# Performance work log

Hardware: AMD Instinct MI355X
Metric: run time of the kernel (lower is better)

The kernel has to match this reference:

```python
import jax, jax.numpy as jnp
import numpy as np

N = 50000   # nodes
E = 800000  # directed edges
D = 128     # input_channels


def _kaiming(key, shape):
    fan_in = shape[0]
    return jax.random.normal(key, shape, jnp.float32) * np.float32(np.sqrt(2.0 / fan_in))


def setup_inputs():
    key = jax.random.key(0)
    ks = jax.random.split(key, 8)
    x = jax.random.normal(ks[0], (N, D), jnp.float32)
    edge_index = jax.random.randint(ks[1], (2, E), 0, N, dtype=jnp.int32)
    return {
        "x": x,
        "edge_index": edge_index,
        "W_in": _kaiming(ks[2], (D, D)),      "b_in": jnp.zeros((D,), jnp.float32),
        "W1": _kaiming(ks[3], (D, 2 * D)),    "b1": jnp.zeros((2 * D,), jnp.float32),
        "W2": _kaiming(ks[4], (2 * D, D)),    "b2": jnp.zeros((D,), jnp.float32),
        "W3": _kaiming(ks[5], (D, D // 2)),   "b3": jnp.zeros((D // 2,), jnp.float32),
        "W_out": _kaiming(ks[6], (D // 2, 1)), "b_out": jnp.zeros((1,), jnp.float32),
    }


def _gcn_conv(x, src, dst, W, b, n):
    """PyG GCNConv: add self-loops, symmetric D^-1/2 (A+I) D^-1/2 normalization."""
    h = x @ W  # [n, out]
    loop = jnp.arange(n, dtype=src.dtype)
    s = jnp.concatenate([src, loop])  # message sources (x_j)
    d = jnp.concatenate([dst, loop])  # aggregation targets (x_i)
    deg = jax.ops.segment_sum(jnp.ones_like(d, jnp.float32), d, num_segments=n)
    dis = jnp.where(deg > 0, jax.lax.rsqrt(jnp.maximum(deg, 1.0)), 0.0)
    norm = dis[s] * dis[d]  # [E+n]
    msg = h[s] * norm[:, None]  # gather + scale
    out = jax.ops.segment_sum(msg, d, num_segments=n)  # scatter-add
    return out + b


def reference(x, edge_index, W_in, b_in, W1, b1, W2, b2, W3, b3, W_out, b_out):
    src, dst = edge_index[0], edge_index[1]
    n = x.shape[0]
    lrelu = lambda t: jax.nn.leaky_relu(t, 0.01)
    # dropout in eval mode (identity)
    h = lrelu(x @ W_in + b_in)
    h = lrelu(_gcn_conv(h, src, dst, W1, b1, n))
    h = lrelu(_gcn_conv(h, src, dst, W2, b2, n))
    h = lrelu(_gcn_conv(h, src, dst, W3, b3, n))
    return h @ W_out + b_out  # [n, 1]
```

## Files before the change

### kernel.cpp

```cpp
#include <hip/hip_runtime.h>
#include <hip/hip_cooperative_groups.h>

namespace cg = cooperative_groups;


#define LRELU(v) ((v) > 0.f ? (v) : 0.01f * (v))

typedef __attribute__((ext_vector_type(8))) _Float16 half8;
typedef __attribute__((ext_vector_type(8))) float float8;
typedef __attribute__((ext_vector_type(4))) float floatx4;

constexpr int CAP = 64;
constexpr int SMEM_H = 16896;

template <int K, int F, int EPI, int CG, int KG, typename IT>
__device__ void phase_gemm(const IT* __restrict__ X,
                           const _Float16* __restrict__ Wt,
                           const float* __restrict__ b,
                           const int* __restrict__ cnt,
                           _Float16* __restrict__ out, int M,
                           _Float16* xs) {
  constexpr int TM = 64;
  constexpr int LK = K + 8;
  constexpr int CW = F / 4;
  constexpr int CPW = CW / CG;
  constexpr int NT = CPW / 16;
  constexpr int KH = K / KG;
  constexpr int NKg = KH / 32;

  const int tid = threadIdx.x;
  const int w = tid >> 6;
  const int lane = tid & 63;
  const int m = lane & 15;
  const int q = lane >> 4;
  const int nTiles = (M + TM - 1) / TM;

  for (int tile = blockIdx.x; tile < nTiles; tile += gridDim.x) {
    const int m0 = tile * TM;
    __syncthreads();
    constexpr int CPR = K / 8;
    for (int idx = tid; idx < TM * CPR; idx += 256) {
      const int row = idx / CPR;
      const int kk = idx % CPR;
      const int g = m0 + row;
      half8 h = (half8)(_Float16)0.f;
      if (g < M) {
        if constexpr (sizeof(IT) == 4) {
          const float4* p = (const float4*)&X[(long)g * K + kk * 8];
          float4 a = p[0], c = p[1];
          h[0] = (_Float16)a.x; h[1] = (_Float16)a.y;
          h[2] = (_Float16)a.z; h[3] = (_Float16)a.w;
          h[4] = (_Float16)c.x; h[5] = (_Float16)c.y;
          h[6] = (_Float16)c.z; h[7] = (_Float16)c.w;
        } else {
          h = *(const half8*)&X[(long)g * K + kk * 8];
        }
      }
      *(half8*)&xs[row * LK + kk * 8] = h;
    }
    __syncthreads();

    for (int cg = 0; cg < CG; ++cg) {
      const int colbase = w * CW + cg * CPW;
      floatx4 acc[4][NT];
#pragma unroll
      for (int rt = 0; rt < 4; ++rt)
#pragma unroll
        for (int t = 0; t < NT; ++t) acc[rt][t] = (floatx4){0.f, 0.f, 0.f, 0.f};

      for (int kg = 0; kg < KG; ++kg) {
        half8 breg[NT][NKg];
#pragma unroll
        for (int t = 0; t < NT; ++t)
#pragma unroll
          for (int kc = 0; kc < NKg; ++kc)
            breg[t][kc] = *(const half8*)&Wt[(long)(colbase + t * 16 + m) * K +
                                             kg * KH + kc * 32 + q * 8];
#pragma unroll
        for (int kc = 0; kc < NKg; ++kc) {
          half8 af[4];
#pragma unroll
          for (int rt = 0; rt < 4; ++rt)
            af[rt] = *(const half8*)&xs[(rt * 16 + m) * LK + kg * KH + kc * 32 +
                                        q * 8];
#pragma unroll
          for (int rt = 0; rt < 4; ++rt)
#pragma unroll
            for (int t = 0; t < NT; ++t)
              acc[rt][t] = __builtin_amdgcn_mfma_f32_16x16x32_f16(
                  af[rt], breg[t][kc], acc[rt][t], 0, 0, 0);
        }
      }

#pragma unroll
      for (int rt = 0; rt < 4; ++rt) {
#pragma unroll
        for (int r = 0; r < 4; ++r) {
          const int row = m0 + rt * 16 + q * 4 + r;
          if (row < M) {
            const float dv = rsqrtf((float)cnt[row] + 1.0f);
#pragma unroll
            for (int t = 0; t < NT; ++t) {
              const int col = colbase + t * 16 + m;
              float v = acc[rt][t][r];
              if constexpr (EPI == 0) { v += b[col]; v = LRELU(v); v *= dv; }
              if constexpr (EPI == 1) { v += b[col]; v = LRELU(v); }
              if constexpr (EPI == 2) { v *= dv; }
              out[(long)row * F + col] = (_Float16)v;
            }
          }
        }
      }
    }
  }
}

template <int F, int MODE>
__device__ void phase_agg(const _Float16* __restrict__ G,
                          const unsigned short* __restrict__ pad,
                          const int* __restrict__ cnt,
                          const float* __restrict__ b,
                          const float* __restrict__ Wout,
                          const float* __restrict__ bout,
                          void* __restrict__ out, int N) {
  const int w = threadIdx.x >> 6;
  const int lane = threadIdx.x & 63;
  const int c = lane & 7;
  const int j = lane >> 3;
  const int n = j >> 2;
  const int jj = j & 3;
  const int uBlk = (N + 7) / 8;
  const int nUnits = (F == 128) ? 2 * uBlk : uBlk;

  for (int u = blockIdx.x; u < nUnits; u += gridDim.x) {
    const int y = (F == 128) ? (u / uBlk) : 0;
    const int ub = (F == 128) ? (u % uBlk) : u;
    int i = ub * 8 + w * 2 + n;
    const bool valid = (i < N);
    if (!valid) i = N - 1;
    const int col0 = y << 6;

    const _Float16* gbase = G + col0 + c * 8;
    const int cn = min(cnt[i], CAP);
    const unsigned short* plist = pad + (long)i * CAP;

    float8 acc = {0.f, 0.f, 0.f, 0.f, 0.f, 0.f, 0.f, 0.f};
    if (jj == 0)
      acc = __builtin_convertvector(*(const half8*)(gbase + (long)i * F), float8);
    for (int e = jj; e < cn; e += 4) {
      const int s = plist[e];
      acc += __builtin_convertvector(*(const half8*)(gbase + (long)s * F), float8);
    }
#pragma unroll
    for (int k = 0; k < 8; ++k) {
      acc[k] += __shfl_xor(acc[k], 8);
      acc[k] += __shfl_xor(acc[k], 16);
    }

    const float dv = rsqrtf((float)cnt[i] + 1.0f);
    if constexpr (MODE == 2) {
      float p = 0.f;
#pragma unroll
      for (int k = 0; k < 8; ++k) {
        const int col = c * 8 + k;
        float v = acc[k] * dv + b[col];
        v = LRELU(v);
        p += v * Wout[col];
      }
      p += __shfl_xor(p, 1);
      p += __shfl_xor(p, 2);
      p += __shfl_xor(p, 4);
      if (valid && jj == 0 && c == 0) ((float*)out)[i] = p + bout[0];
    } else {
      if (valid && jj == 0) {
        half8 hv;
#pragma unroll
        for (int k = 0; k < 8; ++k) {
          float v = acc[k] * dv;
          if constexpr (MODE == 1) { v += b[col0 + c * 8 + k]; v = LRELU(v); }
          hv[k] = (_Float16)v;
        }
        *(half8*)&((_Float16*)out)[(long)i * F + col0 + c * 8] = hv;
      }
    }
  }
}

__global__ __launch_bounds__(256, 4) void k_mega(
    const float* __restrict__ x, const int* __restrict__ src,
    const int* __restrict__ dst, const float* __restrict__ W_in,
    const float* __restrict__ b_in, const float* __restrict__ W1,
    const float* __restrict__ b1, const float* __restrict__ W2,
    const float* __restrict__ b2, const float* __restrict__ W3,
    const float* __restrict__ b3, const float* __restrict__ W_out,
    const float* __restrict__ b_out, int* __restrict__ cnt,
    unsigned short* __restrict__ pad, _Float16* __restrict__ wt_in,
    _Float16* __restrict__ wt1, _Float16* __restrict__ wt2,
    _Float16* __restrict__ wt3, _Float16* __restrict__ buf1,
    _Float16* __restrict__ buf2, _Float16* __restrict__ buf3,
    _Float16* __restrict__ bufg3, float* __restrict__ out,
    int N, int E, int PR) {
  cg::grid_group grid = cg::this_grid();
  __shared__ _Float16 smem[SMEM_H];

  const int tid = threadIdx.x;
  const int b = blockIdx.x;
  const int gid = b * 256 + tid;
  const int GS = gridDim.x * 256;

  for (int i = gid; i < N; i += GS) cnt[i] = 0;
  for (int i = gid; i < 128 * 128; i += GS) {
    const int k = i >> 7, f = i & 127;
    wt_in[f * 128 + k] = (_Float16)W_in[i];
  }
  for (int i = gid; i < 128 * 256; i += GS) {
    const int k = i >> 8, f = i & 255;
    wt1[f * 128 + k] = (_Float16)W1[i];
  }
  for (int i = gid; i < 256 * 128; i += GS) {
    const int k = i >> 7, f = i & 127;
    wt2[f * 256 + k] = (_Float16)W2[i];
  }
  for (int i = gid; i < 128 * 64; i += GS) {
    const int k = i >> 6, f = i & 63;
    wt3[f * 128 + k] = (_Float16)W3[i];
  }
  grid.sync();

  {
    const int range = b & 7;
    const int stride = (gridDim.x >> 3) * 256;
    for (int e = (b >> 3) * 256 + tid; e < E; e += stride) {
      const int d = dst[e];
      if (d / PR == range) {
        const int pos = atomicAdd(&cnt[d], 1);
        if (pos < CAP) pad[(long)d * CAP + pos] = (unsigned short)src[e];
      }
    }
  }
  grid.sync();

  phase_gemm<128, 128, 0, 1, 1, float>(x, wt_in, b_in, cnt, buf1, N, smem);
  grid.sync();
  phase_agg<128, 0>(buf1, pad, cnt, nullptr, nullptr, nullptr, buf2, N);
  grid.sync();
  phase_gemm<128, 256, 1, 2, 1, _Float16>(buf2, wt1, b1, cnt, buf3, N, smem);
  grid.sync();
  phase_gemm<256, 128, 2, 1, 2, _Float16>(buf3, wt2, nullptr, cnt, buf1, N, smem);
  grid.sync();
  phase_agg<128, 1>(buf1, pad, cnt, b2, nullptr, nullptr, buf2, N);
  grid.sync();
  phase_gemm<128, 64, 2, 1, 1, _Float16>(buf2, wt3, nullptr, cnt, bufg3, N, smem);
  grid.sync();
  phase_agg<64, 2>(bufg3, pad, cnt, b3, W_out, b_out, out, N);
}

__global__ __launch_bounds__(256) void k_prep(const int* __restrict__ src,
                                              const int* __restrict__ dst,
                                              int* __restrict__ cnt,
                                              unsigned short* __restrict__ pad,
                                              const float* __restrict__ W_in,
                                              const float* __restrict__ W1,
                                              const float* __restrict__ W2,
                                              const float* __restrict__ W3,
                                              _Float16* __restrict__ wt_in,
                                              _Float16* __restrict__ wt1,
                                              _Float16* __restrict__ wt2,
                                              _Float16* __restrict__ wt3,
                                              int E, int PR) {
  const int b = blockIdx.x;
  const int tid = threadIdx.x;
  if (b < 128) {
    const int m = b >> 5;
    const int idx = (b & 31) * 256 + tid;
    if (m == 0) {
      for (int i = idx; i < 128 * 128; i += 8192) {
        const int k = i >> 7, f = i & 127;
        wt_in[f * 128 + k] = (_Float16)W_in[i];
      }
    } else if (m == 1) {
      for (int i = idx; i < 128 * 256; i += 8192) {
        const int k = i >> 8, f = i & 255;
        wt1[f * 128 + k] = (_Float16)W1[i];
      }
    } else if (m == 2) {
      for (int i = idx; i < 256 * 128; i += 8192) {
        const int k = i >> 7, f = i & 127;
        wt2[f * 256 + k] = (_Float16)W2[i];
      }
    } else {
      for (int i = idx; i < 128 * 64; i += 8192) {
        const int k = i >> 6, f = i & 63;
        wt3[f * 128 + k] = (_Float16)W3[i];
      }
    }
  } else {
    const int bb = b - 128;
    const int range = bb & 7;
    const int e = (bb >> 3) * 256 + tid;
    if (e < E) {
      const int d = dst[e];
      if (d / PR == range) {
        const int pos = atomicAdd(&cnt[d], 1);
        if (pos < CAP) pad[(long)d * CAP + pos] = (unsigned short)src[e];
      }
    }
  }
}

template <int K, int F, int EPI, int CG, int KG, typename IT>
__global__ __launch_bounds__(256) void k_gemm(const IT* __restrict__ X,
                                              const _Float16* __restrict__ Wt,
                                              const float* __restrict__ b,
                                              const int* __restrict__ cnt,
                                              _Float16* __restrict__ out, int M) {
  __shared__ _Float16 smem[64 * (K + 8)];
  phase_gemm<K, F, EPI, CG, KG, IT>(X, Wt, b, cnt, out, M, smem);
}

template <int F, int MODE>
__global__ __launch_bounds__(256) void k_agg(const _Float16* __restrict__ G,
                                             const unsigned short* __restrict__ pad,
                                             const int* __restrict__ cnt,
                                             const float* __restrict__ b,
                                             const float* __restrict__ Wout,
                                             const float* __restrict__ bout,
                                             void* __restrict__ out, int N) {
  phase_agg<F, MODE>(G, pad, cnt, b, Wout, bout, out, N);
}


extern "C" void kernel_launch(void* const* d_in, const int* in_sizes, int n_in,
                              void* d_out, int out_size, void* d_ws, size_t ws_size,
                              hipStream_t stream) {
  const float* x     = (const float*)d_in[0];
  const int* eidx    = (const int*)d_in[1];
  const float* W_in  = (const float*)d_in[2];
  const float* b_in  = (const float*)d_in[3];
  const float* W1    = (const float*)d_in[4];
  const float* b1    = (const float*)d_in[5];
  const float* W2    = (const float*)d_in[6];
  const float* b2    = (const float*)d_in[7];
  const float* W3    = (const float*)d_in[8];
  const float* b3    = (const float*)d_in[9];
  const float* W_out = (const float*)d_in[10];
  const float* b_out = (const float*)d_in[11];
  float* out = (float*)d_out;

  int N = in_sizes[0] / 128;
  int E = in_sizes[1] / 2;
  const int* src = eidx;
  const int* dst = eidx + E;
  int PR = (N + 7) / 8;

  size_t off = 0;
  char* base = (char*)d_ws;
  auto alloc = [&](size_t bytes) -> void* {
    void* p = base + off;
    off = (off + bytes + 255) & ~(size_t)255;
    return p;
  };
  int* cnt            = (int*)alloc((size_t)N * sizeof(int));
  unsigned short* pad = (unsigned short*)alloc((size_t)N * CAP * 2);
  _Float16* wt_in     = (_Float16*)alloc((size_t)128 * 128 * 2);
  _Float16* wt1       = (_Float16*)alloc((size_t)256 * 128 * 2);
  _Float16* wt2       = (_Float16*)alloc((size_t)128 * 256 * 2);
  _Float16* wt3       = (_Float16*)alloc((size_t)64 * 128 * 2);
  _Float16* buf1      = (_Float16*)alloc((size_t)N * 128 * 2);
  _Float16* buf2      = (_Float16*)alloc((size_t)N * 128 * 2);
  _Float16* buf3      = (_Float16*)alloc((size_t)N * 256 * 2);
  _Float16* bufg3     = (_Float16*)alloc((size_t)N * 64 * 2);

  int dev = 0;
  hipGetDevice(&dev);
  int numCU = 0;
  hipDeviceGetAttribute(&numCU, hipDeviceAttributeMultiprocessorCount, dev);
  int maxB = 0;
  hipError_t qe = hipOccupancyMaxActiveBlocksPerMultiprocessor(
      &maxB, (const void*)k_mega, 256, 0);
  int grid = (qe == hipSuccess && numCU > 0) ? maxB * numCU : 0;
  grid &= ~7;
  if (grid > 2048) grid = 2048;

  bool coop = (grid >= 8);
  if (coop) {
    void* kargs[] = {
        (void*)&x,     (void*)&src,  (void*)&dst,   (void*)&W_in,
        (void*)&b_in,  (void*)&W1,   (void*)&b1,    (void*)&W2,
        (void*)&b2,    (void*)&W3,   (void*)&b3,    (void*)&W_out,
        (void*)&b_out, (void*)&cnt,  (void*)&pad,   (void*)&wt_in,
        (void*)&wt1,   (void*)&wt2,  (void*)&wt3,   (void*)&buf1,
        (void*)&buf2,  (void*)&buf3, (void*)&bufg3, (void*)&out,
        (void*)&N,     (void*)&E,    (void*)&PR};
    hipError_t le = hipLaunchCooperativeKernel((const void*)k_mega, dim3(grid),
                                               dim3(256), kargs, 0, stream);
    coop = (le == hipSuccess);
  }

  if (!coop) {
    const int gE = (E + 255) / 256;
    const int gRows = (N + 63) / 64;
    const int gAggP = (N + 7) / 8;
    hipMemsetAsync(cnt, 0, (size_t)N * sizeof(int), stream);
    k_prep<<<128 + 8 * gE, 256, 0, stream>>>(src, dst, cnt, pad, W_in, W1, W2,
                                             W3, wt_in, wt1, wt2, wt3, E, PR);
    k_gemm<128, 128, 0, 1, 1, float><<<gRows, 256, 0, stream>>>(
        x, wt_in, b_in, cnt, buf1, N);
    k_agg<128, 0><<<2 * gAggP, 256, 0, stream>>>(buf1, pad, cnt, nullptr,
                                                 nullptr, nullptr, buf2, N);
    k_gemm<128, 256, 1, 2, 1, _Float16><<<gRows, 256, 0, stream>>>(
        buf2, wt1, b1, cnt, buf3, N);
    k_gemm<256, 128, 2, 1, 2, _Float16><<<gRows, 256, 0, stream>>>(
        buf3, wt2, nullptr, cnt, buf1, N);
    k_agg<128, 1><<<2 * gAggP, 256, 0, stream>>>(buf1, pad, cnt, b2, nullptr,
                                                 nullptr, buf2, N);
    k_gemm<128, 64, 2, 1, 1, _Float16><<<gRows, 256, 0, stream>>>(
        buf2, wt3, nullptr, cnt, bufg3, N);
    k_agg<64, 2><<<gAggP, 256, 0, stream>>>(bufg3, pad, cnt, b3, W_out, b_out,
                                            out, N);
  }
}
```

Baseline: 332.1 us.

## Split K staging in GEMM phase to shrink LDS and raise occupancy

Restructures the GEMM phase so that for K=256 the A tile is staged in two K halves, with accumulators kept across all column groups. Each column group now processes one 16-column MFMA tile at a time, which lowers register pressure. LDS drops to about half, and the megakernel launch bound rises to 5 blocks per CU so more waves stay resident. It also requires a grid of at least 1024 blocks before taking the cooperative path, and otherwise falls back to separate kernels. Costs are extra syncthreads per K split, more weight reloads per column group, and a possible switch to the multi-kernel path on some configurations.

```diff
diff --git a/kernel.cpp b/kernel.cpp
--- a/kernel.cpp
+++ b/kernel.cpp
@@ -11,9 +11,9 @@
 typedef __attribute__((ext_vector_type(4))) float floatx4;
 
 constexpr int CAP = 64;
-constexpr int SMEM_H = 16896;
-
-template <int K, int F, int EPI, int CG, int KG, typename IT>
+constexpr int SMEM_H = 8704;
+
+template <int K, int F, int EPI, int KS, typename IT>
 __device__ void phase_gemm(const IT* __restrict__ X,
                            const _Float16* __restrict__ Wt,
                            const float* __restrict__ b,
@@ -21,11 +21,10 @@
                            _Float16* __restrict__ out, int M,
                            _Float16* xs) {
   constexpr int TM = 64;
-  constexpr int LK = K + 8;
+  constexpr int KH = K / KS;
+  constexpr int LK = KH + 8;
   constexpr int CW = F / 4;
-  constexpr int CPW = CW / CG;
-  constexpr int NT = CPW / 16;
-  constexpr int KH = K / KG;
+  constexpr int CG = CW / 16;
   constexpr int NKg = KH / 32;
 
   const int tid = threadIdx.x;
@@ -37,72 +36,122 @@
 
   for (int tile = blockIdx.x; tile < nTiles; tile += gridDim.x) {
     const int m0 = tile * TM;
-    __syncthreads();
-    constexpr int CPR = K / 8;
-    for (int idx = tid; idx < TM * CPR; idx += 256) {
-      const int row = idx / CPR;
-      const int kk = idx % CPR;
-      const int g = m0 + row;
-      half8 h = (half8)(_Float16)0.f;
-      if (g < M) {
-        if constexpr (sizeof(IT) == 4) {
-          const float4* p = (const float4*)&X[(long)g * K + kk * 8];
-          float4 a = p[0], c = p[1];
-          h[0] = (_Float16)a.x; h[1] = (_Float16)a.y;
-          h[2] = (_Float16)a.z; h[3] = (_Float16)a.w;
-          h[4] = (_Float16)c.x; h[5] = (_Float16)c.y;
-          h[6] = (_Float16)c.z; h[7] = (_Float16)c.w;
-        } else {
-          h = *(const half8*)&X[(long)g * K + kk * 8];
-        }
-      }
-      *(half8*)&xs[row * LK + kk * 8] = h;
-    }
-    __syncthreads();
-
-    for (int cg = 0; cg < CG; ++cg) {
-      const int colbase = w * CW + cg * CPW;
-      floatx4 acc[4][NT];
-#pragma unroll
-      for (int rt = 0; rt < 4; ++rt)
-#pragma unroll
-        for (int t = 0; t < NT; ++t) acc[rt][t] = (floatx4){0.f, 0.f, 0.f, 0.f};
-
-      for (int kg = 0; kg < KG; ++kg) {
-        half8 breg[NT][NKg];
-#pragma unroll
-        for (int t = 0; t < NT; ++t)
-#pragma unroll
-          for (int kc = 0; kc < NKg; ++kc)
-            breg[t][kc] = *(const half8*)&Wt[(long)(colbase + t * 16 + m) * K +
-                                             kg * KH + kc * 32 + q * 8];
+
+    if constexpr (KS == 1) {
+      __syncthreads();
+      constexpr int CPR = KH / 8;
+      for (int idx = tid; idx < TM * CPR; idx += 256) {
+        const int row = idx / CPR;
+        const int kk = idx % CPR;
+        const int g = m0 + row;
+        half8 h = (half8)(_Float16)0.f;
+        if (g < M) {
+          if constexpr (sizeof(IT) == 4) {
+            const float4* p = (const float4*)&X[(long)g * K + kk * 8];
+            float4 a = p[0], c = p[1];
+            h[0] = (_Float16)a.x; h[1] = (_Float16)a.y;
+            h[2] = (_Float16)a.z; h[3] = (_Float16)a.w;
+            h[4] = (_Float16)c.x; h[5] = (_Float16)c.y;
+            h[6] = (_Float16)c.z; h[7] = (_Float16)c.w;
+          } else {
+            h = *(const half8*)&X[(long)g * K + kk * 8];
+          }
+        }
+        *(half8*)&xs[row * LK + kk * 8] = h;
+      }
+      __syncthreads();
+
+      for (int cg = 0; cg < CG; ++cg) {
+        const int colbase = w * CW + cg * 16;
+        half8 breg[NKg];
+#pragma unroll
+        for (int kc = 0; kc < NKg; ++kc)
+          breg[kc] =
+              *(const half8*)&Wt[(long)(colbase + m) * K + kc * 32 + q * 8];
+        floatx4 acc[4];
+#pragma unroll
+        for (int rt = 0; rt < 4; ++rt) acc[rt] = (floatx4){0.f, 0.f, 0.f, 0.f};
 #pragma unroll
         for (int kc = 0; kc < NKg; ++kc) {
           half8 af[4];
 #pragma unroll
           for (int rt = 0; rt < 4; ++rt)
-            af[rt] = *(const half8*)&xs[(rt * 16 + m) * LK + kg * KH + kc * 32 +
-                                        q * 8];
+            af[rt] = *(const half8*)&xs[(rt * 16 + m) * LK + kc * 32 + q * 8];
 #pragma unroll
           for (int rt = 0; rt < 4; ++rt)
-#pragma unroll
-            for (int t = 0; t < NT; ++t)
-              acc[rt][t] = __builtin_amdgcn_mfma_f32_16x16x32_f16(
-                  af[rt], breg[t][kc], acc[rt][t], 0, 0, 0);
-        }
-      }
-
-#pragma unroll
-      for (int rt = 0; rt < 4; ++rt) {
-#pragma unroll
-        for (int r = 0; r < 4; ++r) {
-          const int row = m0 + rt * 16 + q * 4 + r;
-          if (row < M) {
-            const float dv = rsqrtf((float)cnt[row] + 1.0f);
-#pragma unroll
-            for (int t = 0; t < NT; ++t) {
-              const int col = colbase + t * 16 + m;
-              float v = acc[rt][t][r];
+            acc[rt] = __builtin_amdgcn_mfma_f32_16x16x32_f16(af[rt], breg[kc],
+                                                             acc[rt], 0, 0, 0);
+        }
+#pragma unroll
+        for (int rt = 0; rt < 4; ++rt) {
+#pragma unroll
+          for (int r = 0; r < 4; ++r) {
+            const int row = m0 + rt * 16 + q * 4 + r;
+            if (row < M) {
+              const float dv = rsqrtf((float)cnt[row] + 1.0f);
+              const int col = colbase + m;
+              float v = acc[rt][r];
+              if constexpr (EPI == 0) { v += b[col]; v = LRELU(v); v *= dv; }
+              if constexpr (EPI == 1) { v += b[col]; v = LRELU(v); }
+              if constexpr (EPI == 2) { v *= dv; }
+              out[(long)row * F + col] = (_Float16)v;
+            }
+          }
+        }
+      }
+    } else {
+      floatx4 acc[CG][4];
+#pragma unroll
+      for (int cg = 0; cg < CG; ++cg)
+#pragma unroll
+        for (int rt = 0; rt < 4; ++rt) acc[cg][rt] = (floatx4){0.f, 0.f, 0.f, 0.f};
+
+      for (int ks = 0; ks < KS; ++ks) {
+        __syncthreads();
+        constexpr int CPR = KH / 8;
+        for (int idx = tid; idx < TM * CPR; idx += 256) {
+          const int row = idx / CPR;
+          const int kk = idx % CPR;
+          const int g = m0 + row;
+          half8 h = (half8)(_Float16)0.f;
+          if (g < M) h = *(const half8*)&X[(long)g * K + ks * KH + kk * 8];
+          *(half8*)&xs[row * LK + kk * 8] = h;
+        }
+        __syncthreads();
+
+        for (int cg = 0; cg < CG; ++cg) {
+          const int colbase = w * CW + cg * 16;
+          half8 breg[NKg];
+#pragma unroll
+          for (int kc = 0; kc < NKg; ++kc)
+            breg[kc] = *(const half8*)&Wt[(long)(colbase + m) * K + ks * KH +
+                                          kc * 32 + q * 8];
+#pragma unroll
+          for (int kc = 0; kc < NKg; ++kc) {
+            half8 af[4];
+#pragma unroll
+            for (int rt = 0; rt < 4; ++rt)
+              af[rt] = *(const half8*)&xs[(rt * 16 + m) * LK + kc * 32 + q * 8];
+#pragma unroll
+            for (int rt = 0; rt < 4; ++rt)
+              acc[cg][rt] = __builtin_amdgcn_mfma_f32_16x16x32_f16(
+                  af[rt], breg[kc], acc[cg][rt], 0, 0, 0);
+          }
+        }
+      }
+
+#pragma unroll
+      for (int cg = 0; cg < CG; ++cg) {
+        const int colbase = w * CW + cg * 16;
+#pragma unroll
+        for (int rt = 0; rt < 4; ++rt) {
+#pragma unroll
+          for (int r = 0; r < 4; ++r) {
+            const int row = m0 + rt * 16 + q * 4 + r;
+            if (row < M) {
+              const float dv = rsqrtf((float)cnt[row] + 1.0f);
+              const int col = colbase + m;
+              float v = acc[cg][rt][r];
               if constexpr (EPI == 0) { v += b[col]; v = LRELU(v); v *= dv; }
               if constexpr (EPI == 1) { v += b[col]; v = LRELU(v); }
               if constexpr (EPI == 2) { v *= dv; }
@@ -186,7 +235,7 @@
   }
 }
 
-__global__ __launch_bounds__(256, 4) void k_mega(
+__global__ __launch_bounds__(256, 5) void k_mega(
     const float* __restrict__ x, const int* __restrict__ src,
     const int* __restrict__ dst, const float* __restrict__ W_in,
     const float* __restrict__ b_in, const float* __restrict__ W1,
@@ -240,17 +289,17 @@
   }
   grid.sync();
 
-  phase_gemm<128, 128, 0, 1, 1, float>(x, wt_in, b_in, cnt, buf1, N, smem);
+  phase_gemm<128, 128, 0, 1, float>(x, wt_in, b_in, cnt, buf1, N, smem);
   grid.sync();
   phase_agg<128, 0>(buf1, pad, cnt, nullptr, nullptr, nullptr, buf2, N);
   grid.sync();
-  phase_gemm<128, 256, 1, 2, 1, _Float16>(buf2, wt1, b1, cnt, buf3, N, smem);
-  grid.sync();
-  phase_gemm<256, 128, 2, 1, 2, _Float16>(buf3, wt2, nullptr, cnt, buf1, N, smem);
+  phase_gemm<128, 256, 1, 1, _Float16>(buf2, wt1, b1, cnt, buf3, N, smem);
+  grid.sync();
+  phase_gemm<256, 128, 2, 2, _Float16>(buf3, wt2, nullptr, cnt, buf1, N, smem);
   grid.sync();
   phase_agg<128, 1>(buf1, pad, cnt, b2, nullptr, nullptr, buf2, N);
   grid.sync();
-  phase_gemm<128, 64, 2, 1, 1, _Float16>(buf2, wt3, nullptr, cnt, bufg3, N, smem);
+  phase_gemm<128, 64, 2, 1, _Float16>(buf2, wt3, nullptr, cnt, bufg3, N, smem);
   grid.sync();
   phase_agg<64, 2>(bufg3, pad, cnt, b3, W_out, b_out, out, N);
 }
@@ -308,14 +357,14 @@
   }
 }
 
-template <int K, int F, int EPI, int CG, int KG, typename IT>
+template <int K, int F, int EPI, int KS, typename IT>
 __global__ __launch_bounds__(256) void k_gemm(const IT* __restrict__ X,
                                               const _Float16* __restrict__ Wt,
                                               const float* __restrict__ b,
                                               const int* __restrict__ cnt,
                                               _Float16* __restrict__ out, int M) {
-  __shared__ _Float16 smem[64 * (K + 8)];
-  phase_gemm<K, F, EPI, CG, KG, IT>(X, Wt, b, cnt, out, M, smem);
+  __shared__ _Float16 smem[64 * (K / KS + 8)];
+  phase_gemm<K, F, EPI, KS, IT>(X, Wt, b, cnt, out, M, smem);
 }
 
 template <int F, int MODE>
@@ -382,7 +431,7 @@
   grid &= ~7;
   if (grid > 2048) grid = 2048;
 
-  bool coop = (grid >= 8);
+  bool coop = (grid >= 1024);
   if (coop) {
     void* kargs[] = {
         (void*)&x,     (void*)&src,  (void*)&dst,   (void*)&W_in,
@@ -404,17 +453,17 @@
     hipMemsetAsync(cnt, 0, (size_t)N * sizeof(int), stream);
     k_prep<<<128 + 8 * gE, 256, 0, stream>>>(src, dst, cnt, pad, W_in, W1, W2,
                                              W3, wt_in, wt1, wt2, wt3, E, PR);
-    k_gemm<128, 128, 0, 1, 1, float><<<gRows, 256, 0, stream>>>(
+    k_gemm<128, 128, 0, 1, float><<<gRows, 256, 0, stream>>>(
         x, wt_in, b_in, cnt, buf1, N);
     k_agg<128, 0><<<2 * gAggP, 256, 0, stream>>>(buf1, pad, cnt, nullptr,
                                                  nullptr, nullptr, buf2, N);
-    k_gemm<128, 256, 1, 2, 1, _Float16><<<gRows, 256, 0, stream>>>(
+    k_gemm<128, 256, 1, 1, _Float16><<<gRows, 256, 0, stream>>>(
         buf2, wt1, b1, cnt, buf3, N);
-    k_gemm<256, 128, 2, 1, 2, _Float16><<<gRows, 256, 0, stream>>>(
+    k_gemm<256, 128, 2, 2, _Float16><<<gRows, 256, 0, stream>>>(
         buf3, wt2, nullptr, cnt, buf1, N);
     k_agg<128, 1><<<2 * gAggP, 256, 0, stream>>>(buf1, pad, cnt, b2, nullptr,
                                                  nullptr, buf2, N);
-    k_gemm<128, 64, 2, 1, 1, _Float16><<<gRows, 256, 0, stream>>>(
+    k_gemm<128, 64, 2, 1, _Float16><<<gRows, 256, 0, stream>>>(
         buf2, wt3, nullptr, cnt, bufg3, N);
     k_agg<64, 2><<<gAggP, 256, 0, stream>>>(bufg3, pad, cnt, b3, W_out, b_out,
                                             out, N);
```

Measured after the change: 331.3 us. Within noise of the previous version (-0.2%).
